# Kernel tuning notes

Measured on AMD Instinct MI355X. Metric: run time of the kernel, lower is better.

## Reference

```python
import jax, jax.numpy as jnp
import numpy as np

B, T, N, IN_DIM = 32, 12, 1024, 1
HID, EMB, K, HOR, OUT = 64, 16, 2, 12, 1


def setup_inputs() -> dict:
    key = jax.random.key(0)
    ks = jax.random.split(key, 12)
    s = 0.1
    return {
        "x": jax.random.normal(ks[0], (B, T, N, IN_DIM), jnp.float32),
        "E": jax.random.normal(ks[1], (N, EMB), jnp.float32),
        # layer 1: gate (z,r) and candidate pools; in = IN_DIM + HID
        "Wg1": jax.random.normal(ks[2], (EMB, K, IN_DIM + HID, 2 * HID), jnp.float32) * s,
        "bg1": jax.random.normal(ks[3], (EMB, 2 * HID), jnp.float32) * s,
        "Wc1": jax.random.normal(ks[4], (EMB, K, IN_DIM + HID, HID), jnp.float32) * s,
        "bc1": jax.random.normal(ks[5], (EMB, HID), jnp.float32) * s,
        # layer 2: in = HID + HID
        "Wg2": jax.random.normal(ks[6], (EMB, K, 2 * HID, 2 * HID), jnp.float32) * s,
        "bg2": jax.random.normal(ks[7], (EMB, 2 * HID), jnp.float32) * s,
        "Wc2": jax.random.normal(ks[8], (EMB, K, 2 * HID, HID), jnp.float32) * s,
        "bc2": jax.random.normal(ks[9], (EMB, HID), jnp.float32) * s,
        # Conv2d(1, HOR*OUT, kernel=(1, HID)) == per-node linear HID -> HOR*OUT
        "Wout": jax.random.normal(ks[10], (HOR * OUT, HID), jnp.float32) * s,
        "bout": jnp.zeros((HOR * OUT,), jnp.float32),
    }


def _supports(E):
    # adaptive adjacency from node embeddings + Chebyshev polynomial set
    A = jax.nn.softmax(jax.nn.relu(E @ E.T), axis=1)  # [N, N]
    sup = [jnp.eye(E.shape[0], dtype=E.dtype), A]
    for _ in range(K - 2):
        sup.append(2.0 * (A @ sup[-1]) - sup[-2])
    return jnp.stack(sup[:K])  # [K, N, N]


def _gconv(x, sup, E, Wp, bp):
    # x: [B, N, Ci]; per-node weights generated from embeddings
    xg = jnp.einsum('knm,bmc->bnkc', sup, x)          # [B, N, K, Ci]
    W = jnp.einsum('nd,dkio->nkio', E, Wp)            # [N, K, Ci, Co]
    b = E @ bp                                        # [N, Co]
    return jnp.einsum('bnki,nkio->bno', xg, W) + b


def _layer(xs, sup, E, Wg, bg, Wc, bc):
    # xs: [T, B, N, Ci]; adaptive graph-conv GRU scanned over time
    hid = Wc.shape[-1]

    def step(h, x_t):
        zr = jax.nn.sigmoid(_gconv(jnp.concatenate([x_t, h], -1), sup, E, Wg, bg))
        z, r = jnp.split(zr, 2, axis=-1)
        hc = jnp.tanh(_gconv(jnp.concatenate([x_t, z * h], -1), sup, E, Wc, bc))
        h_new = r * h + (1.0 - r) * hc
        return h_new, h_new

    h0 = jnp.zeros((xs.shape[1], xs.shape[2], hid), xs.dtype)
    _, hs = jax.lax.scan(step, h0, xs)
    return hs  # [T, B, N, hid]


def reference(x, E, Wg1, bg1, Wc1, bc1, Wg2, bg2, Wc2, bc2, Wout, bout):
    sup = _supports(E)
    xs = jnp.swapaxes(x, 0, 1)                        # [T, B, N, in]
    h1 = _layer(xs, sup, E, Wg1, bg1, Wc1, bc1)       # [T, B, N, HID]
    h2 = _layer(h1, sup, E, Wg2, bg2, Wc2, bc2)       # [T, B, N, HID]
    h_last = h2[-1]                                   # [B, N, HID]
    out = jnp.einsum('bnh,oh->bno', h_last, Wout) + bout  # [B, N, HOR*OUT]
    out = jnp.transpose(out, (0, 2, 1)).reshape(x.shape[0], HOR, OUT, N)
    return jnp.transpose(out, (0, 1, 3, 2))           # [B, HOR, N, OUT]
```

## Files before the change

kernel.cpp:

```cpp
#include <hip/hip_runtime.h>
#include <math.h>

#define NN 1024
#define BB 32
#define TTT 12
#define HH 64
#define DD 16

__device__ __forceinline__ float dot4f(const float4 v, const float* __restrict__ wv) {
    return v.x * wv[0] + v.y * wv[1] + v.z * wv[2] + v.w * wv[3];
}

__device__ __forceinline__ float sigmoidf_(float x) { return 1.0f / (1.0f + expf(-x)); }

__global__ __launch_bounds__(256) void compute_A_kernel(const float* __restrict__ E,
                                                        float* __restrict__ A) {
    int n = blockIdx.x;
    int tid = threadIdx.x;
    __shared__ float en[DD];
    __shared__ float red[256];
    if (tid < DD) en[tid] = E[n * DD + tid];
    __syncthreads();
    float s[4];
    float lmax = 0.0f;
    #pragma unroll
    for (int it = 0; it < 4; ++it) {
        int m = tid + it * 256;
        float acc = 0.0f;
        #pragma unroll
        for (int d = 0; d < DD; ++d) acc += en[d] * E[m * DD + d];
        acc = fmaxf(acc, 0.0f);
        s[it] = acc;
        lmax = fmaxf(lmax, acc);
    }
    red[tid] = lmax; __syncthreads();
    for (int st = 128; st > 0; st >>= 1) {
        if (tid < st) red[tid] = fmaxf(red[tid], red[tid + st]);
        __syncthreads();
    }
    float mx = red[0];
    __syncthreads();
    float lsum = 0.0f;
    #pragma unroll
    for (int it = 0; it < 4; ++it) { s[it] = expf(s[it] - mx); lsum += s[it]; }
    red[tid] = lsum; __syncthreads();
    for (int st = 128; st > 0; st >>= 1) {
        if (tid < st) red[tid] += red[tid + st];
        __syncthreads();
    }
    float inv = 1.0f / red[0];
    #pragma unroll
    for (int it = 0; it < 4; ++it) {
        int m = tid + it * 256;
        A[n * NN + m] = s[it] * inv;
    }
}

__global__ __launch_bounds__(256) void gen_w_f32_kernel(const float* __restrict__ E,
                                                        const float* __restrict__ Wp,
                                                        float* __restrict__ out,
                                                        int rowlen, int total) {
    int idx = blockIdx.x * 256 + threadIdx.x;
    if (idx >= total) return;
    int n = idx / rowlen;
    int j = idx - n * rowlen;
    const float* e = E + n * DD;
    float acc = 0.0f;
    #pragma unroll
    for (int d = 0; d < DD; ++d) acc += e[d] * Wp[d * rowlen + j];
    out[idx] = acc;
}

__global__ __launch_bounds__(256) void gen_w4_kernel(const float* __restrict__ E,
                                                     const float4* __restrict__ Wp4,
                                                     float4* __restrict__ out4,
                                                     int rowlen4, int total4) {
    int idx = blockIdx.x * 256 + threadIdx.x;
    if (idx >= total4) return;
    int n = idx / rowlen4;
    int j = idx - n * rowlen4;
    const float* e = E + n * DD;
    float4 acc = make_float4(0.f, 0.f, 0.f, 0.f);
    #pragma unroll
    for (int d = 0; d < DD; ++d) {
        float ed = e[d];
        float4 w = Wp4[(size_t)d * rowlen4 + j];
        acc.x += ed * w.x; acc.y += ed * w.y; acc.z += ed * w.z; acc.w += ed * w.w;
    }
    out4[idx] = acc;
}

__global__ __launch_bounds__(256) void transpose_x_kernel(const float* __restrict__ x,
                                                          float* __restrict__ xTm) {
    int idx = blockIdx.x * 256 + threadIdx.x;
    int m = idx / (TTT * BB);
    int tb = idx - m * (TTT * BB);
    int t = tb >> 5;
    int b = tb & 31;
    xTm[idx] = x[(b * TTT + t) * NN + m];
}

__global__ __launch_bounds__(256) void diffuse_gemm(const float* __restrict__ A,
                                                    const float* __restrict__ S,
                                                    float* __restrict__ C, int cols) {
    __shared__ alignas(16) float As[2][16][68];
    __shared__ alignas(16) float Bs[2][16][64];
    const int tid = threadIdx.x;
    const int tx = tid & 15, ty = tid >> 4;
    const int rowbase = blockIdx.y * 64, colbase = blockIdx.x * 64;
    const int kl = tid & 15, r0 = (tid >> 4) * 4;
    const int ml = tid >> 6, cl = tid & 63;
    float pa[4], pb[4];
    #pragma unroll
    for (int r = 0; r < 4; ++r)
        pa[r] = A[(size_t)(rowbase + r0 + r) * NN + kl];
    #pragma unroll
    for (int mm = 0; mm < 4; ++mm)
        pb[mm] = S[(size_t)(ml + mm * 4) * cols + colbase + cl];
    #pragma unroll
    for (int r = 0; r < 4; ++r) As[0][kl][r0 + r] = pa[r];
    #pragma unroll
    for (int mm = 0; mm < 4; ++mm) Bs[0][ml + mm * 4][cl] = pb[mm];
    __syncthreads();
    int cur = 0;
    float acc[4][4] = {};
    for (int kt = 0; kt < NN; kt += 16) {
        int kn = kt + 16;
        if (kn < NN) {
            #pragma unroll
            for (int r = 0; r < 4; ++r)
                pa[r] = A[(size_t)(rowbase + r0 + r) * NN + kn + kl];
            #pragma unroll
            for (int mm = 0; mm < 4; ++mm)
                pb[mm] = S[(size_t)(kn + ml + mm * 4) * cols + colbase + cl];
        }
        #pragma unroll
        for (int kk = 0; kk < 16; ++kk) {
            float4 a = *(const float4*)&As[cur][kk][ty * 4];
            float4 b = *(const float4*)&Bs[cur][kk][tx * 4];
            acc[0][0] += a.x * b.x; acc[0][1] += a.x * b.y; acc[0][2] += a.x * b.z; acc[0][3] += a.x * b.w;
            acc[1][0] += a.y * b.x; acc[1][1] += a.y * b.y; acc[1][2] += a.y * b.z; acc[1][3] += a.y * b.w;
            acc[2][0] += a.z * b.x; acc[2][1] += a.z * b.y; acc[2][2] += a.z * b.z; acc[2][3] += a.z * b.w;
            acc[3][0] += a.w * b.x; acc[3][1] += a.w * b.y; acc[3][2] += a.w * b.z; acc[3][3] += a.w * b.w;
        }
        if (kn < NN) {
            int nxt = cur ^ 1;
            #pragma unroll
            for (int r = 0; r < 4; ++r) As[nxt][kl][r0 + r] = pa[r];
            #pragma unroll
            for (int mm = 0; mm < 4; ++mm) Bs[nxt][ml + mm * 4][cl] = pb[mm];
            __syncthreads();
            cur = nxt;
        }
    }
    #pragma unroll
    for (int i = 0; i < 4; ++i) {
        float4 v = make_float4(acc[i][0], acc[i][1], acc[i][2], acc[i][3]);
        *(float4*)&C[(size_t)(rowbase + ty * 4 + i) * cols + colbase + tx * 4] = v;
    }
}


__global__ __launch_bounds__(256) void l1_gate_kernel(int t,
        const float* __restrict__ xTm, const float* __restrict__ AxA,
        const float* __restrict__ h1, const float* __restrict__ Ah1,
        const float* __restrict__ Wg, const float* __restrict__ Bg,
        float* __restrict__ zh, float* __restrict__ rb) {
    int n = blockIdx.x;
    int tid = threadIdx.x;
    __shared__ alignas(16) float sh[BB * HH];
    __shared__ alignas(16) float sa[BB * HH];
    __shared__ float sx[BB], sax[BB];
    for (int i = tid; i < BB * HH; i += 256) {
        sh[i] = h1[(size_t)n * (BB * HH) + i];
        sa[i] = Ah1[(size_t)n * (BB * HH) + i];
    }
    if (tid < BB) sx[tid] = xTm[n * (TTT * BB) + t * BB + tid];
    else if (tid < 2 * BB) sax[tid - BB] = AxA[n * (TTT * BB) + t * BB + (tid - BB)];
    __syncthreads();
    const int o = tid & 63;
    const int bq = tid >> 6;
    const float* W = Wg + (size_t)n * 16640;
    float accA[8], accB[8];
    float biasA = Bg[n * 128 + o], biasB = Bg[n * 128 + 64 + o];
    float wxa0 = W[o], wxa1 = W[8320 + o];
    float wxb0 = W[64 + o], wxb1 = W[8320 + 64 + o];
    #pragma unroll
    for (int j = 0; j < 8; ++j) {
        int b = bq * 8 + j;
        accA[j] = biasA + sx[b] * wxa0 + sax[b] * wxa1;
        accB[j] = biasB + sx[b] * wxb0 + sax[b] * wxb1;
    }
    for (int i = 0; i < HH; i += 4) {
        float w0a[4], w1a[4], w0b[4], w1b[4];
        #pragma unroll
        for (int q = 0; q < 4; ++q) {
            int row = (1 + i + q) * 128;
            w0a[q] = W[row + o];            w1a[q] = W[8320 + row + o];
            w0b[q] = W[row + 64 + o];       w1b[q] = W[8320 + row + 64 + o];
        }
        #pragma unroll
        for (int j = 0; j < 8; ++j) {
            int b = bq * 8 + j;
            float4 hv = *(const float4*)&sh[b * HH + i];
            float4 av = *(const float4*)&sa[b * HH + i];
            accA[j] += dot4f(hv, w0a) + dot4f(av, w1a);
            accB[j] += dot4f(hv, w0b) + dot4f(av, w1b);
        }
    }
    #pragma unroll
    for (int j = 0; j < 8; ++j) {
        int b = bq * 8 + j;
        float z = sigmoidf_(accA[j]);
        float r = sigmoidf_(accB[j]);
        zh[(size_t)n * (BB * HH) + b * HH + o] = z * sh[b * HH + o];
        rb[(size_t)n * (BB * HH) + b * HH + o] = r;
    }
}

__global__ __launch_bounds__(256) void l2_gate_kernel(
        const float* __restrict__ h1, const float* __restrict__ Ah1,
        const float* __restrict__ h2, const float* __restrict__ Ah2,
        const float* __restrict__ Wg, const float* __restrict__ Bg,
        float* __restrict__ zh, float* __restrict__ rb) {
    int n = blockIdx.x;
    int tid = threadIdx.x;
    __shared__ alignas(16) float s1[BB * HH];
    __shared__ alignas(16) float sa1[BB * HH];
    __shared__ alignas(16) float s2[BB * HH];
    __shared__ alignas(16) float sa2[BB * HH];
    for (int i = tid; i < BB * HH; i += 256) {
        size_t base = (size_t)n * (BB * HH) + i;
        s1[i] = h1[base]; sa1[i] = Ah1[base];
        s2[i] = h2[base]; sa2[i] = Ah2[base];
    }
    __syncthreads();
    const int o = tid & 63;
    const int bq = tid >> 6;
    const float* W = Wg + (size_t)n * 32768;
    float accA[8], accB[8];
    float biasA = Bg[n * 128 + o], biasB = Bg[n * 128 + 64 + o];
    #pragma unroll
    for (int j = 0; j < 8; ++j) { accA[j] = biasA; accB[j] = biasB; }
    for (int i = 0; i < HH; i += 4) {
        float w10a[4], w11a[4], w20a[4], w21a[4];
        float w10b[4], w11b[4], w20b[4], w21b[4];
        #pragma unroll
        for (int q = 0; q < 4; ++q) {
            int r1 = (i + q) * 128;
            int r2 = (64 + i + q) * 128;
            w10a[q] = W[r1 + o];          w10b[q] = W[r1 + 64 + o];
            w11a[q] = W[16384 + r1 + o];  w11b[q] = W[16384 + r1 + 64 + o];
            w20a[q] = W[r2 + o];          w20b[q] = W[r2 + 64 + o];
            w21a[q] = W[16384 + r2 + o];  w21b[q] = W[16384 + r2 + 64 + o];
        }
        #pragma unroll
        for (int j = 0; j < 8; ++j) {
            int b = bq * 8 + j;
            float4 v1 = *(const float4*)&s1[b * HH + i];
            float4 u1 = *(const float4*)&sa1[b * HH + i];
            float4 v2 = *(const float4*)&s2[b * HH + i];
            float4 u2 = *(const float4*)&sa2[b * HH + i];
            accA[j] += dot4f(v1, w10a) + dot4f(u1, w11a) + dot4f(v2, w20a) + dot4f(u2, w21a);
            accB[j] += dot4f(v1, w10b) + dot4f(u1, w11b) + dot4f(v2, w20b) + dot4f(u2, w21b);
        }
    }
    #pragma unroll
    for (int j = 0; j < 8; ++j) {
        int b = bq * 8 + j;
        float z = sigmoidf_(accA[j]);
        float r = sigmoidf_(accB[j]);
        zh[(size_t)n * (BB * HH) + b * HH + o] = z * s2[b * HH + o];
        rb[(size_t)n * (BB * HH) + b * HH + o] = r;
    }
}


__global__ __launch_bounds__(256) void l1_gate_fused(int t,
        const float* __restrict__ xTm, const float* __restrict__ AxA,
        const float* __restrict__ h1, const float* __restrict__ Ah1,
        const float* __restrict__ E, const float4* __restrict__ Wp4,
        const float* __restrict__ Bg,
        float* __restrict__ zh, float* __restrict__ rb) {
    int n = blockIdx.x, tid = threadIdx.x;
    __shared__ float en[DD];
    __shared__ alignas(16) float Wl[65 * 128];
    __shared__ alignas(16) float S0[BB * HH];
    __shared__ alignas(16) float S1[BB * HH];
    __shared__ float sx[BB], sax[BB];
    if (tid < DD) en[tid] = E[n * DD + tid];
    for (int i = tid; i < BB * HH; i += 256) {
        S0[i] = h1[(size_t)n * (BB * HH) + i];
        S1[i] = Ah1[(size_t)n * (BB * HH) + i];
    }
    if (tid < BB) sx[tid] = xTm[n * (TTT * BB) + t * BB + tid];
    else if (tid < 2 * BB) sax[tid - BB] = AxA[n * (TTT * BB) + t * BB + (tid - BB)];
    __syncthreads();
    const int o = tid & 63, bq = tid >> 6;
    float accA[8], accB[8];
    float biasA = Bg[n * 128 + o], biasB = Bg[n * 128 + 64 + o];
    #pragma unroll
    for (int j = 0; j < 8; ++j) { accA[j] = biasA; accB[j] = biasB; }
    for (int k = 0; k < 2; ++k) {
        for (int idx = tid; idx < 2080; idx += 256) {
            float4 a = make_float4(0.f, 0.f, 0.f, 0.f);
            #pragma unroll
            for (int d = 0; d < DD; ++d) {
                float ed = en[d];
                float4 w = Wp4[(size_t)d * 4160 + k * 2080 + idx];
                a.x += ed * w.x; a.y += ed * w.y; a.z += ed * w.z; a.w += ed * w.w;
            }
            *(float4*)&Wl[idx * 4] = a;
        }
        __syncthreads();
        const float* S = (k == 0) ? S0 : S1;
        float wxa = Wl[o], wxb = Wl[64 + o];
        #pragma unroll
        for (int j = 0; j < 8; ++j) {
            int b = bq * 8 + j;
            float xv = (k == 0) ? sx[b] : sax[b];
            accA[j] += xv * wxa; accB[j] += xv * wxb;
        }
        for (int i = 0; i < HH; i += 4) {
            float wa[4], wb[4];
            #pragma unroll
            for (int q = 0; q < 4; ++q) {
                int row = (1 + i + q) * 128;
                wa[q] = Wl[row + o]; wb[q] = Wl[row + 64 + o];
            }
            #pragma unroll
            for (int j = 0; j < 8; ++j) {
                int b = bq * 8 + j;
                float4 sv = *(const float4*)&S[b * HH + i];
                accA[j] += dot4f(sv, wa); accB[j] += dot4f(sv, wb);
            }
        }
        __syncthreads();
    }
    #pragma unroll
    for (int j = 0; j < 8; ++j) {
        int b = bq * 8 + j;
        float z = sigmoidf_(accA[j]);
        float r = sigmoidf_(accB[j]);
        zh[(size_t)n * (BB * HH) + b * HH + o] = z * S0[b * HH + o];
        rb[(size_t)n * (BB * HH) + b * HH + o] = r;
    }
}

__global__ __launch_bounds__(256) void l1_cand_fused(int t,
        const float* __restrict__ xTm, const float* __restrict__ AxA,
        const float* __restrict__ zhb, const float* __restrict__ azh,
        const float* __restrict__ E, const float4* __restrict__ Wp4,
        const float* __restrict__ Bc,
        const float* __restrict__ rb, float* __restrict__ h1) {
    int n = blockIdx.x, tid = threadIdx.x;
    __shared__ float en[DD];
    __shared__ alignas(16) float Wl[65 * 64];
    __shared__ alignas(16) float S0[BB * HH];
    __shared__ alignas(16) float S1[BB * HH];
    __shared__ float sx[BB], sax[BB];
    if (tid < DD) en[tid] = E[n * DD + tid];
    for (int i = tid; i < BB * HH; i += 256) {
        S0[i] = zhb[(size_t)n * (BB * HH) + i];
        S1[i] = azh[(size_t)n * (BB * HH) + i];
    }
    if (tid < BB) sx[tid] = xTm[n * (TTT * BB) + t * BB + tid];
    else if (tid < 2 * BB) sax[tid - BB] = AxA[n * (TTT * BB) + t * BB + (tid - BB)];
    __syncthreads();
    const int o = tid & 63, bq = tid >> 6;
    float acc[8];
    float bias = Bc[n * 64 + o];
    #pragma unroll
    for (int j = 0; j < 8; ++j) acc[j] = bias;
    for (int k = 0; k < 2; ++k) {
        for (int idx = tid; idx < 1040; idx += 256) {
            float4 a = make_float4(0.f, 0.f, 0.f, 0.f);
            #pragma unroll
            for (int d = 0; d < DD; ++d) {
                float ed = en[d];
                float4 w = Wp4[(size_t)d * 2080 + k * 1040 + idx];
                a.x += ed * w.x; a.y += ed * w.y; a.z += ed * w.z; a.w += ed * w.w;
            }
            *(float4*)&Wl[idx * 4] = a;
        }
        __syncthreads();
        const float* S = (k == 0) ? S0 : S1;
        float wx = Wl[o];
        #pragma unroll
        for (int j = 0; j < 8; ++j) {
            int b = bq * 8 + j;
            float xv = (k == 0) ? sx[b] : sax[b];
            acc[j] += xv * wx;
        }
        for (int i = 0; i < HH; i += 4) {
            float wa[4];
            #pragma unroll
            for (int q = 0; q < 4; ++q) wa[q] = Wl[(1 + i + q) * 64 + o];
            #pragma unroll
            for (int j = 0; j < 8; ++j) {
                int b = bq * 8 + j;
                float4 sv = *(const float4*)&S[b * HH + i];
                acc[j] += dot4f(sv, wa);
            }
        }
        __syncthreads();
    }
    #pragma unroll
    for (int j = 0; j < 8; ++j) {
        int b = bq * 8 + j;
        size_t idx = (size_t)n * (BB * HH) + b * HH + o;
        float hc = tanhf(acc[j]);
        float r = rb[idx];
        float hold = h1[idx];
        h1[idx] = r * hold + (1.0f - r) * hc;
    }
}

__global__ __launch_bounds__(256) void l2_cand_fused(
        const float* __restrict__ h1, const float* __restrict__ Ah1,
        const float* __restrict__ zhb, const float* __restrict__ azh,
        const float* __restrict__ E, const float4* __restrict__ Wp4,
        const float* __restrict__ Bc,
        const float* __restrict__ rb, float* __restrict__ h2) {
    int n = blockIdx.x, tid = threadIdx.x;
    __shared__ float en[DD];
    __shared__ alignas(16) float Wl[64 * 64];
    __shared__ alignas(16) float Sl[4][BB * HH];
    if (tid < DD) en[tid] = E[n * DD + tid];
    for (int i = tid; i < BB * HH; i += 256) {
        size_t base = (size_t)n * (BB * HH) + i;
        Sl[0][i] = h1[base];  Sl[1][i] = zhb[base];
        Sl[2][i] = Ah1[base]; Sl[3][i] = azh[base];
    }
    __syncthreads();
    const int o = tid & 63, bq = tid >> 6;
    float acc[8];
    float bias = Bc[n * 64 + o];
    #pragma unroll
    for (int j = 0; j < 8; ++j) acc[j] = bias;
    for (int p = 0; p < 4; ++p) {
        int k = p >> 1, half = p & 1;
        for (int idx = tid; idx < 1024; idx += 256) {
            float4 a = make_float4(0.f, 0.f, 0.f, 0.f);
            #pragma unroll
            for (int d = 0; d < DD; ++d) {
                float ed = en[d];
                float4 w = Wp4[(size_t)d * 4096 + k * 2048 + half * 1024 + idx];
                a.x += ed * w.x; a.y += ed * w.y; a.z += ed * w.z; a.w += ed * w.w;
            }
            *(float4*)&Wl[idx * 4] = a;
        }
        __syncthreads();
        const float* S = Sl[k * 2 + half];
        for (int i = 0; i < HH; i += 4) {
            float wa[4];
            #pragma unroll
            for (int qq = 0; qq < 4; ++qq) wa[qq] = Wl[(i + qq) * 64 + o];
            #pragma unroll
            for (int j = 0; j < 8; ++j) {
                int b = bq * 8 + j;
                float4 sv = *(const float4*)&S[b * HH + i];
                acc[j] += dot4f(sv, wa);
            }
        }
        __syncthreads();
    }
    #pragma unroll
    for (int j = 0; j < 8; ++j) {
        int b = bq * 8 + j;
        size_t idx = (size_t)n * (BB * HH) + b * HH + o;
        float hc = tanhf(acc[j]);
        float r = rb[idx];
        float hold = h2[idx];
        h2[idx] = r * hold + (1.0f - r) * hc;
    }
}

__global__ __launch_bounds__(384) void out_kernel(const float* __restrict__ h2,
                                                  const float* __restrict__ Wout,
                                                  const float* __restrict__ bout,
                                                  float* __restrict__ out) {
    int n = blockIdx.x;
    int tid = threadIdx.x;
    __shared__ float shh[BB * HH];
    __shared__ float sw[TTT * HH];
    __shared__ float sb[TTT];
    for (int i = tid; i < BB * HH; i += 384) shh[i] = h2[(size_t)n * (BB * HH) + i];
    for (int i = tid; i < TTT * HH; i += 384) sw[i] = Wout[i];
    if (tid < TTT) sb[tid] = bout[tid];
    __syncthreads();
    int b = tid & 31;
    int hor = tid >> 5;
    float acc = sb[hor];
    #pragma unroll
    for (int c = 0; c < HH; ++c) acc += shh[b * HH + c] * sw[hor * HH + c];
    out[(size_t)(b * TTT + hor) * NN + n] = acc;
}

__global__ void report_ws_kernel(float* out, float v) { out[0] = v; }

extern "C" void kernel_launch(void* const* d_in, const int* in_sizes, int n_in,
                              void* d_out, int out_size, void* d_ws, size_t ws_size,
                              hipStream_t stream) {
    const float* x    = (const float*)d_in[0];
    const float* E    = (const float*)d_in[1];
    const float* Wg1p = (const float*)d_in[2];
    const float* bg1p = (const float*)d_in[3];
    const float* Wc1p = (const float*)d_in[4];
    const float* bc1p = (const float*)d_in[5];
    const float* Wg2p = (const float*)d_in[6];
    const float* bg2p = (const float*)d_in[7];
    const float* Wc2p = (const float*)d_in[8];
    const float* bc2p = (const float*)d_in[9];
    const float* Wout = (const float*)d_in[10];
    const float* bout = (const float*)d_in[11];
    float* out = (float*)d_out;
    float* ws = (float*)d_ws;

    size_t off = 0;
    float* A_   = ws + off; off += (size_t)NN * NN;
    float* B1g  = ws + off; off += (size_t)NN * 128;
    float* B1c  = ws + off; off += (size_t)NN * 64;
    float* B2g  = ws + off; off += (size_t)NN * 128;
    float* B2c  = ws + off; off += (size_t)NN * 64;
    float* xTm  = ws + off; off += (size_t)NN * TTT * BB;
    float* AxA  = ws + off; off += (size_t)NN * TTT * BB;
    const size_t ST = (size_t)NN * BB * HH;
    float* h1   = ws + off; off += ST;
    float* h2   = ws + off; off += ST;
    float* Ah1  = ws + off; off += ST;
    float* Ah2  = ws + off; off += ST;
    float* Azh  = ws + off; off += ST;
    float* ZH   = ws + off; off += ST;
    float* Rb   = ws + off; off += ST;
    float* W2G  = ws + off; off += (size_t)NN * 32768;
    size_t need_w2g = off * sizeof(float);
    float* W1G  = ws + off;
    size_t need_w1g = need_w2g + (size_t)NN * 16640 * sizeof(float);
    if (ws_size < need_w2g) {
        report_ws_kernel<<<1, 1, 0, stream>>>(out, (float)ws_size);
        return;
    }
    const bool w1g_static = (ws_size >= need_w1g);

    (void)hipMemsetAsync(h1, 0, ST * 4, stream);
    (void)hipMemsetAsync(h2, 0, ST * 4, stream);
    (void)hipMemsetAsync(Ah1, 0, ST * 4, stream);
    (void)hipMemsetAsync(Ah2, 0, ST * 4, stream);
    (void)hipMemsetAsync(Azh, 0, ST * 4, stream);

    compute_A_kernel<<<NN, 256, 0, stream>>>(E, A_);
    gen_w_f32_kernel<<<(131072 + 255) / 256, 256, 0, stream>>>(E, bg1p, B1g, 128, 131072);
    gen_w_f32_kernel<<<(65536 + 255) / 256, 256, 0, stream>>>(E, bc1p, B1c, 64, 65536);
    gen_w_f32_kernel<<<(131072 + 255) / 256, 256, 0, stream>>>(E, bg2p, B2g, 128, 131072);
    gen_w_f32_kernel<<<(65536 + 255) / 256, 256, 0, stream>>>(E, bc2p, B2c, 64, 65536);
    transpose_x_kernel<<<(NN * TTT * BB) / 256, 256, 0, stream>>>(x, xTm);
    diffuse_gemm<<<dim3((TTT * BB) / 64, NN / 64), 256, 0, stream>>>(A_, xTm, AxA, TTT * BB);
    gen_w4_kernel<<<(8388608 + 255) / 256, 256, 0, stream>>>(
        E, (const float4*)Wg2p, (float4*)W2G, 8192, 8388608);
    if (w1g_static) {
        gen_w4_kernel<<<(4259840 + 255) / 256, 256, 0, stream>>>(
            E, (const float4*)Wg1p, (float4*)W1G, 4160, 4259840);
    }

    const int COLS = BB * HH;
    dim3 gemmGrid(COLS / 64, NN / 64);

    for (int t = 0; t < TTT; ++t) {
        if (w1g_static)
            l1_gate_kernel<<<NN, 256, 0, stream>>>(t, xTm, AxA, h1, Ah1, W1G, B1g, ZH, Rb);
        else
            l1_gate_fused<<<NN, 256, 0, stream>>>(t, xTm, AxA, h1, Ah1,
                                                  E, (const float4*)Wg1p, B1g, ZH, Rb);
        if (t > 0) diffuse_gemm<<<gemmGrid, 256, 0, stream>>>(A_, ZH, Azh, COLS);
        l1_cand_fused<<<NN, 256, 0, stream>>>(t, xTm, AxA, ZH, Azh,
                                              E, (const float4*)Wc1p, B1c, Rb, h1);
        diffuse_gemm<<<gemmGrid, 256, 0, stream>>>(A_, h1, Ah1, COLS);
        l2_gate_kernel<<<NN, 256, 0, stream>>>(h1, Ah1, h2, Ah2, W2G, B2g, ZH, Rb);
        if (t > 0) diffuse_gemm<<<gemmGrid, 256, 0, stream>>>(A_, ZH, Azh, COLS);
        l2_cand_fused<<<NN, 256, 0, stream>>>(h1, Ah1, ZH, Azh,
                                              E, (const float4*)Wc2p, B2c, Rb, h2);
        if (t < TTT - 1) diffuse_gemm<<<gemmGrid, 256, 0, stream>>>(A_, h2, Ah2, COLS);
    }

    out_kernel<<<NN, 384, 0, stream>>>(h2, Wout, bout, out);
}
```

Before: 5.891 ms.

## Stage per-node weights through LDS, precompute layer-1 candidate weights, shrink GEMM tile

New measurement: 6.782 ms. 1.15x slower.

```diff
diff --git a/kernel.cpp b/kernel.cpp
--- a/kernel.cpp
+++ b/kernel.cpp
@@ -103,50 +103,48 @@
 __global__ __launch_bounds__(256) void diffuse_gemm(const float* __restrict__ A,
                                                     const float* __restrict__ S,
                                                     float* __restrict__ C, int cols) {
-    __shared__ alignas(16) float As[2][16][68];
+    __shared__ alignas(16) float As[2][16][36];
     __shared__ alignas(16) float Bs[2][16][64];
     const int tid = threadIdx.x;
     const int tx = tid & 15, ty = tid >> 4;
-    const int rowbase = blockIdx.y * 64, colbase = blockIdx.x * 64;
-    const int kl = tid & 15, r0 = (tid >> 4) * 4;
+    const int rowbase = blockIdx.y * 32, colbase = blockIdx.x * 64;
+    const int kl = tid & 15, r2 = (tid >> 4) * 2;
     const int ml = tid >> 6, cl = tid & 63;
-    float pa[4], pb[4];
-    #pragma unroll
-    for (int r = 0; r < 4; ++r)
-        pa[r] = A[(size_t)(rowbase + r0 + r) * NN + kl];
+    float pa[2], pb[4];
+    #pragma unroll
+    for (int r = 0; r < 2; ++r)
+        pa[r] = A[(size_t)(rowbase + r2 + r) * NN + kl];
     #pragma unroll
     for (int mm = 0; mm < 4; ++mm)
         pb[mm] = S[(size_t)(ml + mm * 4) * cols + colbase + cl];
     #pragma unroll
-    for (int r = 0; r < 4; ++r) As[0][kl][r0 + r] = pa[r];
+    for (int r = 0; r < 2; ++r) As[0][kl][r2 + r] = pa[r];
     #pragma unroll
     for (int mm = 0; mm < 4; ++mm) Bs[0][ml + mm * 4][cl] = pb[mm];
     __syncthreads();
     int cur = 0;
-    float acc[4][4] = {};
+    float acc[2][4] = {};
     for (int kt = 0; kt < NN; kt += 16) {
         int kn = kt + 16;
         if (kn < NN) {
             #pragma unroll
-            for (int r = 0; r < 4; ++r)
-                pa[r] = A[(size_t)(rowbase + r0 + r) * NN + kn + kl];
+            for (int r = 0; r < 2; ++r)
+                pa[r] = A[(size_t)(rowbase + r2 + r) * NN + kn + kl];
             #pragma unroll
             for (int mm = 0; mm < 4; ++mm)
                 pb[mm] = S[(size_t)(kn + ml + mm * 4) * cols + colbase + cl];
         }
         #pragma unroll
         for (int kk = 0; kk < 16; ++kk) {
-            float4 a = *(const float4*)&As[cur][kk][ty * 4];
+            float2 a = *(const float2*)&As[cur][kk][ty * 2];
             float4 b = *(const float4*)&Bs[cur][kk][tx * 4];
             acc[0][0] += a.x * b.x; acc[0][1] += a.x * b.y; acc[0][2] += a.x * b.z; acc[0][3] += a.x * b.w;
             acc[1][0] += a.y * b.x; acc[1][1] += a.y * b.y; acc[1][2] += a.y * b.z; acc[1][3] += a.y * b.w;
-            acc[2][0] += a.z * b.x; acc[2][1] += a.z * b.y; acc[2][2] += a.z * b.z; acc[2][3] += a.z * b.w;
-            acc[3][0] += a.w * b.x; acc[3][1] += a.w * b.y; acc[3][2] += a.w * b.z; acc[3][3] += a.w * b.w;
         }
         if (kn < NN) {
             int nxt = cur ^ 1;
             #pragma unroll
-            for (int r = 0; r < 4; ++r) As[nxt][kl][r0 + r] = pa[r];
+            for (int r = 0; r < 2; ++r) As[nxt][kl][r2 + r] = pa[r];
             #pragma unroll
             for (int mm = 0; mm < 4; ++mm) Bs[nxt][ml + mm * 4][cl] = pb[mm];
             __syncthreads();
@@ -154,124 +152,180 @@
         }
     }
     #pragma unroll
-    for (int i = 0; i < 4; ++i) {
+    for (int i = 0; i < 2; ++i) {
         float4 v = make_float4(acc[i][0], acc[i][1], acc[i][2], acc[i][3]);
-        *(float4*)&C[(size_t)(rowbase + ty * 4 + i) * cols + colbase + tx * 4] = v;
-    }
-}
-
-
-__global__ __launch_bounds__(256) void l1_gate_kernel(int t,
+        *(float4*)&C[(size_t)(rowbase + ty * 2 + i) * cols + colbase + tx * 4] = v;
+    }
+}
+
+
+__global__ __launch_bounds__(256) void l1_gate_staged(int t,
         const float* __restrict__ xTm, const float* __restrict__ AxA,
         const float* __restrict__ h1, const float* __restrict__ Ah1,
         const float* __restrict__ Wg, const float* __restrict__ Bg,
         float* __restrict__ zh, float* __restrict__ rb) {
-    int n = blockIdx.x;
-    int tid = threadIdx.x;
-    __shared__ alignas(16) float sh[BB * HH];
-    __shared__ alignas(16) float sa[BB * HH];
+    int n = blockIdx.x, tid = threadIdx.x;
+    __shared__ alignas(16) float Wl[65 * 128];
+    __shared__ alignas(16) float S0[BB * HH];
+    __shared__ alignas(16) float S1[BB * HH];
     __shared__ float sx[BB], sax[BB];
     for (int i = tid; i < BB * HH; i += 256) {
-        sh[i] = h1[(size_t)n * (BB * HH) + i];
-        sa[i] = Ah1[(size_t)n * (BB * HH) + i];
+        S0[i] = h1[(size_t)n * (BB * HH) + i];
+        S1[i] = Ah1[(size_t)n * (BB * HH) + i];
     }
     if (tid < BB) sx[tid] = xTm[n * (TTT * BB) + t * BB + tid];
     else if (tid < 2 * BB) sax[tid - BB] = AxA[n * (TTT * BB) + t * BB + (tid - BB)];
-    __syncthreads();
-    const int o = tid & 63;
-    const int bq = tid >> 6;
-    const float* W = Wg + (size_t)n * 16640;
+    const int o = tid & 63, bq = tid >> 6;
     float accA[8], accB[8];
     float biasA = Bg[n * 128 + o], biasB = Bg[n * 128 + 64 + o];
-    float wxa0 = W[o], wxa1 = W[8320 + o];
-    float wxb0 = W[64 + o], wxb1 = W[8320 + 64 + o];
-    #pragma unroll
-    for (int j = 0; j < 8; ++j) {
-        int b = bq * 8 + j;
-        accA[j] = biasA + sx[b] * wxa0 + sax[b] * wxa1;
-        accB[j] = biasB + sx[b] * wxb0 + sax[b] * wxb1;
-    }
-    for (int i = 0; i < HH; i += 4) {
-        float w0a[4], w1a[4], w0b[4], w1b[4];
-        #pragma unroll
-        for (int q = 0; q < 4; ++q) {
-            int row = (1 + i + q) * 128;
-            w0a[q] = W[row + o];            w1a[q] = W[8320 + row + o];
-            w0b[q] = W[row + 64 + o];       w1b[q] = W[8320 + row + 64 + o];
-        }
+    #pragma unroll
+    for (int j = 0; j < 8; ++j) { accA[j] = biasA; accB[j] = biasB; }
+    for (int k = 0; k < 2; ++k) {
+        const float4* src = (const float4*)(Wg + (size_t)n * 16640 + k * 8320);
+        for (int idx = tid; idx < 2080; idx += 256)
+            ((float4*)Wl)[idx] = src[idx];
+        __syncthreads();
+        const float* S = (k == 0) ? S0 : S1;
+        float wxa = Wl[o], wxb = Wl[64 + o];
         #pragma unroll
         for (int j = 0; j < 8; ++j) {
             int b = bq * 8 + j;
-            float4 hv = *(const float4*)&sh[b * HH + i];
-            float4 av = *(const float4*)&sa[b * HH + i];
-            accA[j] += dot4f(hv, w0a) + dot4f(av, w1a);
-            accB[j] += dot4f(hv, w0b) + dot4f(av, w1b);
-        }
+            float xv = (k == 0) ? sx[b] : sax[b];
+            accA[j] += xv * wxa; accB[j] += xv * wxb;
+        }
+        for (int i = 0; i < HH; i += 4) {
+            float wa[4], wb[4];
+            #pragma unroll
+            for (int q = 0; q < 4; ++q) {
+                int row = (1 + i + q) * 128;
+                wa[q] = Wl[row + o]; wb[q] = Wl[row + 64 + o];
+            }
+            #pragma unroll
+            for (int j = 0; j < 8; ++j) {
+                int b = bq * 8 + j;
+                float4 sv = *(const float4*)&S[b * HH + i];
+                accA[j] += dot4f(sv, wa); accB[j] += dot4f(sv, wb);
+            }
+        }
+        __syncthreads();
     }
     #pragma unroll
     for (int j = 0; j < 8; ++j) {
         int b = bq * 8 + j;
         float z = sigmoidf_(accA[j]);
         float r = sigmoidf_(accB[j]);
-        zh[(size_t)n * (BB * HH) + b * HH + o] = z * sh[b * HH + o];
+        zh[(size_t)n * (BB * HH) + b * HH + o] = z * S0[b * HH + o];
         rb[(size_t)n * (BB * HH) + b * HH + o] = r;
     }
 }
 
-__global__ __launch_bounds__(256) void l2_gate_kernel(
+__global__ __launch_bounds__(256) void l2_gate_staged(
         const float* __restrict__ h1, const float* __restrict__ Ah1,
         const float* __restrict__ h2, const float* __restrict__ Ah2,
         const float* __restrict__ Wg, const float* __restrict__ Bg,
         float* __restrict__ zh, float* __restrict__ rb) {
-    int n = blockIdx.x;
-    int tid = threadIdx.x;
-    __shared__ alignas(16) float s1[BB * HH];
-    __shared__ alignas(16) float sa1[BB * HH];
-    __shared__ alignas(16) float s2[BB * HH];
-    __shared__ alignas(16) float sa2[BB * HH];
+    int n = blockIdx.x, tid = threadIdx.x;
+    __shared__ alignas(16) float Wl[32 * 128];
+    __shared__ alignas(16) float Sl[4][BB * HH];
     for (int i = tid; i < BB * HH; i += 256) {
         size_t base = (size_t)n * (BB * HH) + i;
-        s1[i] = h1[base]; sa1[i] = Ah1[base];
-        s2[i] = h2[base]; sa2[i] = Ah2[base];
-    }
-    __syncthreads();
-    const int o = tid & 63;
-    const int bq = tid >> 6;
-    const float* W = Wg + (size_t)n * 32768;
+        Sl[0][i] = h1[base]; Sl[1][i] = h2[base];
+        Sl[2][i] = Ah1[base]; Sl[3][i] = Ah2[base];
+    }
+    const int o = tid & 63, bq = tid >> 6;
     float accA[8], accB[8];
     float biasA = Bg[n * 128 + o], biasB = Bg[n * 128 + 64 + o];
     #pragma unroll
     for (int j = 0; j < 8; ++j) { accA[j] = biasA; accB[j] = biasB; }
-    for (int i = 0; i < HH; i += 4) {
-        float w10a[4], w11a[4], w20a[4], w21a[4];
-        float w10b[4], w11b[4], w20b[4], w21b[4];
-        #pragma unroll
-        for (int q = 0; q < 4; ++q) {
-            int r1 = (i + q) * 128;
-            int r2 = (64 + i + q) * 128;
-            w10a[q] = W[r1 + o];          w10b[q] = W[r1 + 64 + o];
-            w11a[q] = W[16384 + r1 + o];  w11b[q] = W[16384 + r1 + 64 + o];
-            w20a[q] = W[r2 + o];          w20b[q] = W[r2 + 64 + o];
-            w21a[q] = W[16384 + r2 + o];  w21b[q] = W[16384 + r2 + 64 + o];
-        }
-        #pragma unroll
-        for (int j = 0; j < 8; ++j) {
-            int b = bq * 8 + j;
-            float4 v1 = *(const float4*)&s1[b * HH + i];
-            float4 u1 = *(const float4*)&sa1[b * HH + i];
-            float4 v2 = *(const float4*)&s2[b * HH + i];
-            float4 u2 = *(const float4*)&sa2[b * HH + i];
-            accA[j] += dot4f(v1, w10a) + dot4f(u1, w11a) + dot4f(v2, w20a) + dot4f(u2, w21a);
-            accB[j] += dot4f(v1, w10b) + dot4f(u1, w11b) + dot4f(v2, w20b) + dot4f(u2, w21b);
-        }
+    for (int p = 0; p < 8; ++p) {
+        int k = p >> 2, q = p & 3;
+        const float4* src = (const float4*)(Wg + (size_t)n * 32768 + k * 16384 + q * 4096);
+        for (int idx = tid; idx < 1024; idx += 256)
+            ((float4*)Wl)[idx] = src[idx];
+        __syncthreads();
+        const float* S = Sl[k * 2 + (q >> 1)];
+        int ibase = (q & 1) * 32;
+        for (int i = 0; i < 32; i += 4) {
+            float wa[4], wb[4];
+            #pragma unroll
+            for (int qq = 0; qq < 4; ++qq) {
+                wa[qq] = Wl[(i + qq) * 128 + o];
+                wb[qq] = Wl[(i + qq) * 128 + 64 + o];
+            }
+            #pragma unroll
+            for (int j = 0; j < 8; ++j) {
+                int b = bq * 8 + j;
+                float4 sv = *(const float4*)&S[b * HH + ibase + i];
+                accA[j] += dot4f(sv, wa); accB[j] += dot4f(sv, wb);
+            }
+        }
+        __syncthreads();
     }
     #pragma unroll
     for (int j = 0; j < 8; ++j) {
         int b = bq * 8 + j;
         float z = sigmoidf_(accA[j]);
         float r = sigmoidf_(accB[j]);
-        zh[(size_t)n * (BB * HH) + b * HH + o] = z * s2[b * HH + o];
+        zh[(size_t)n * (BB * HH) + b * HH + o] = z * Sl[1][b * HH + o];
         rb[(size_t)n * (BB * HH) + b * HH + o] = r;
+    }
+}
+
+__global__ __launch_bounds__(256) void l1_cand_staged(int t,
+        const float* __restrict__ xTm, const float* __restrict__ AxA,
+        const float* __restrict__ zhb, const float* __restrict__ azh,
+        const float* __restrict__ Wc, const float* __restrict__ Bc,
+        const float* __restrict__ rb, float* __restrict__ h1) {
+    int n = blockIdx.x, tid = threadIdx.x;
+    __shared__ alignas(16) float Wl[65 * 64];
+    __shared__ alignas(16) float S0[BB * HH];
+    __shared__ alignas(16) float S1[BB * HH];
+    __shared__ float sx[BB], sax[BB];
+    for (int i = tid; i < BB * HH; i += 256) {
+        S0[i] = zhb[(size_t)n * (BB * HH) + i];
+        S1[i] = azh[(size_t)n * (BB * HH) + i];
+    }
+    if (tid < BB) sx[tid] = xTm[n * (TTT * BB) + t * BB + tid];
+    else if (tid < 2 * BB) sax[tid - BB] = AxA[n * (TTT * BB) + t * BB + (tid - BB)];
+    const int o = tid & 63, bq = tid >> 6;
+    float acc[8];
+    float bias = Bc[n * 64 + o];
+    #pragma unroll
+    for (int j = 0; j < 8; ++j) acc[j] = bias;
+    for (int k = 0; k < 2; ++k) {
+        const float4* src = (const float4*)(Wc + (size_t)n * 8320 + k * 4160);
+        for (int idx = tid; idx < 1040; idx += 256)
+            ((float4*)Wl)[idx] = src[idx];
+        __syncthreads();
+        const float* S = (k == 0) ? S0 : S1;
+        float wx = Wl[o];
+        #pragma unroll
+        for (int j = 0; j < 8; ++j) {
+            int b = bq * 8 + j;
+            float xv = (k == 0) ? sx[b] : sax[b];
+            acc[j] += xv * wx;
+        }
+        for (int i = 0; i < HH; i += 4) {
+            float wa[4];
+            #pragma unroll
+            for (int q = 0; q < 4; ++q) wa[q] = Wl[(1 + i + q) * 64 + o];
+            #pragma unroll
+            for (int j = 0; j < 8; ++j) {
+                int b = bq * 8 + j;
+                float4 sv = *(const float4*)&S[b * HH + i];
+                acc[j] += dot4f(sv, wa);
+            }
+        }
+        __syncthreads();
+    }
+    #pragma unroll
+    for (int j = 0; j < 8; ++j) {
+        int b = bq * 8 + j;
+        size_t idx = (size_t)n * (BB * HH) + b * HH + o;
+        float hc = tanhf(acc[j]);
+        float r = rb[idx];
+        float hold = h1[idx];
+        h1[idx] = r * hold + (1.0f - r) * hc;
     }
 }
 
@@ -537,11 +591,14 @@
     size_t need_w2g = off * sizeof(float);
     float* W1G  = ws + off;
     size_t need_w1g = need_w2g + (size_t)NN * 16640 * sizeof(float);
+    float* W1C  = ws + off + (size_t)NN * 16640;
+    size_t need_w1c = need_w1g + (size_t)NN * 8320 * sizeof(float);
     if (ws_size < need_w2g) {
         report_ws_kernel<<<1, 1, 0, stream>>>(out, (float)ws_size);
         return;
     }
     const bool w1g_static = (ws_size >= need_w1g);
+    const bool w1c_static = (ws_size >= need_w1c);
 
     (void)hipMemsetAsync(h1, 0, ST * 4, stream);
     (void)hipMemsetAsync(h2, 0, ST * 4, stream);
@@ -555,28 +612,35 @@
     gen_w_f32_kernel<<<(131072 + 255) / 256, 256, 0, stream>>>(E, bg2p, B2g, 128, 131072);
     gen_w_f32_kernel<<<(65536 + 255) / 256, 256, 0, stream>>>(E, bc2p, B2c, 64, 65536);
     transpose_x_kernel<<<(NN * TTT * BB) / 256, 256, 0, stream>>>(x, xTm);
-    diffuse_gemm<<<dim3((TTT * BB) / 64, NN / 64), 256, 0, stream>>>(A_, xTm, AxA, TTT * BB);
+    diffuse_gemm<<<dim3((TTT * BB) / 64, NN / 32), 256, 0, stream>>>(A_, xTm, AxA, TTT * BB);
     gen_w4_kernel<<<(8388608 + 255) / 256, 256, 0, stream>>>(
         E, (const float4*)Wg2p, (float4*)W2G, 8192, 8388608);
     if (w1g_static) {
         gen_w4_kernel<<<(4259840 + 255) / 256, 256, 0, stream>>>(
             E, (const float4*)Wg1p, (float4*)W1G, 4160, 4259840);
     }
+    if (w1c_static) {
+        gen_w4_kernel<<<(2129920 + 255) / 256, 256, 0, stream>>>(
+            E, (const float4*)Wc1p, (float4*)W1C, 2080, 2129920);
+    }
 
     const int COLS = BB * HH;
-    dim3 gemmGrid(COLS / 64, NN / 64);
+    dim3 gemmGrid(COLS / 64, NN / 32);
 
     for (int t = 0; t < TTT; ++t) {
         if (w1g_static)
-            l1_gate_kernel<<<NN, 256, 0, stream>>>(t, xTm, AxA, h1, Ah1, W1G, B1g, ZH, Rb);
+            l1_gate_staged<<<NN, 256, 0, stream>>>(t, xTm, AxA, h1, Ah1, W1G, B1g, ZH, Rb);
         else
             l1_gate_fused<<<NN, 256, 0, stream>>>(t, xTm, AxA, h1, Ah1,
                                                   E, (const float4*)Wg1p, B1g, ZH, Rb);
         if (t > 0) diffuse_gemm<<<gemmGrid, 256, 0, stream>>>(A_, ZH, Azh, COLS);
-        l1_cand_fused<<<NN, 256, 0, stream>>>(t, xTm, AxA, ZH, Azh,
-                                              E, (const float4*)Wc1p, B1c, Rb, h1);
+        if (w1c_static)
+            l1_cand_staged<<<NN, 256, 0, stream>>>(t, xTm, AxA, ZH, Azh, W1C, B1c, Rb, h1);
+        else
+            l1_cand_fused<<<NN, 256, 0, stream>>>(t, xTm, AxA, ZH, Azh,
+                                                  E, (const float4*)Wc1p, B1c, Rb, h1);
         diffuse_gemm<<<gemmGrid, 256, 0, stream>>>(A_, h1, Ah1, COLS);
-        l2_gate_kernel<<<NN, 256, 0, stream>>>(h1, Ah1, h2, Ah2, W2G, B2g, ZH, Rb);
+        l2_gate_staged<<<NN, 256, 0, stream>>>(h1, Ah1, h2, Ah2, W2G, B2g, ZH, Rb);
         if (t > 0) diffuse_gemm<<<gemmGrid, 256, 0, stream>>>(A_, ZH, Azh, COLS);
         l2_cand_fused<<<NN, 256, 0, stream>>>(h1, Ah1, ZH, Azh,
                                               E, (const float4*)Wc2p, B2c, Rb, h2);
```
